# Performance work log

Measured on AMD Instinct MI355X. Metric: run time of the kernel, lower is better.

The kernel has to match this reference:

```python
import jax, jax.numpy as jnp
import numpy as np

TEMPERATURE = 0.5
B, D = 4096, 256

def setup_inputs() -> dict:
    key = jax.random.key(0)
    k1, k2 = jax.random.split(key)
    z_i = jax.random.normal(k1, (B, D), dtype=jnp.float32)
    z_j = jax.random.normal(k2, (B, D), dtype=jnp.float32)
    return {"z_i": z_i, "z_j": z_j}

def reference(z_i, z_j):
    # NT-Xent loss (SimCLR). Cosine similarity of L2-normalized rows == dot product.
    b = z_i.shape[0]
    n = 2 * b
    zi = z_i / jnp.linalg.norm(z_i, axis=1, keepdims=True)
    zj = z_j / jnp.linalg.norm(z_j, axis=1, keepdims=True)
    z = jnp.concatenate([zi, zj], axis=0)            # [N, D]
    sim = jnp.matmul(z, z.T)                          # [N, N] cosine-sim matrix
    # positives: sim(i, i+b) and sim(i+b, i)
    pos = jnp.concatenate([jnp.diagonal(sim, offset=b), jnp.diagonal(sim, offset=-b)])  # [N]
    logits = sim / TEMPERATURE
    # Cross-entropy with the positive as the target class over {pos} U negatives.
    # The candidate set per row is all j != i (the positive j = partner(i) is included,
    # only the self-similarity diagonal is excluded) -> mask diagonal with -inf.
    neg_inf = jnp.asarray(-jnp.inf, dtype=logits.dtype)
    masked = jnp.where(jnp.eye(n, dtype=bool), neg_inf, logits)
    lse = jax.nn.logsumexp(masked, axis=1)            # [N]
    loss = jnp.sum(lse - pos / TEMPERATURE) / n
    return loss
```

## Files before the change

### kernel.cpp

```cpp
#include <hip/hip_runtime.h>
#include <hip/hip_bf16.h>


constexpr int BB = 4096;
constexpr int NN = 8192;
constexpr int DD = 256;
constexpr int TS = 128;
constexpr int NT = NN / TS;
constexpr int NBLK = NT * (NT + 1) / 2;
constexpr int KCH = 64;
constexpr int NCH = DD / KCH;

typedef _Float16 half4v __attribute__((ext_vector_type(4)));
typedef _Float16 half8v __attribute__((ext_vector_type(8)));
typedef float floatx16 __attribute__((ext_vector_type(16)));

__global__ __launch_bounds__(256) void nt_normalize(
    const float* __restrict__ zi, const float* __restrict__ zj,
    _Float16* __restrict__ Z, float* __restrict__ posPartial,
    float* __restrict__ rowsum)
{
    const int lane = threadIdx.x & 63;
    const int wave = threadIdx.x >> 6;
    const int i = blockIdx.x * 4 + wave;

    if (blockIdx.x < 32) rowsum[blockIdx.x * 256 + threadIdx.x] = 0.f;

    const float4 a = ((const float4*)(zi + (size_t)i * DD))[lane];
    const float4 b = ((const float4*)(zj + (size_t)i * DD))[lane];

    float ssi = a.x*a.x + a.y*a.y + a.z*a.z + a.w*a.w;
    float ssj = b.x*b.x + b.y*b.y + b.z*b.z + b.w*b.w;
    float dd  = a.x*b.x + a.y*b.y + a.z*b.z + a.w*b.w;
#pragma unroll
    for (int off = 32; off > 0; off >>= 1) {
        ssi += __shfl_xor(ssi, off);
        ssj += __shfl_xor(ssj, off);
        dd  += __shfl_xor(dd,  off);
    }
    const float invi = rsqrtf(ssi);
    const float invj = rsqrtf(ssj);

    half4v ha, hb;
    ha.x = (_Float16)(a.x * invi); ha.y = (_Float16)(a.y * invi);
    ha.z = (_Float16)(a.z * invi); ha.w = (_Float16)(a.w * invi);
    hb.x = (_Float16)(b.x * invj); hb.y = (_Float16)(b.y * invj);
    hb.z = (_Float16)(b.z * invj); hb.w = (_Float16)(b.w * invj);

    ((half4v*)(Z + (size_t)i * DD))[lane]        = ha;
    ((half4v*)(Z + (size_t)(BB + i) * DD))[lane] = hb;

    __shared__ float ps[4];
    if (lane == 0) ps[wave] = dd * invi * invj;
    __syncthreads();
    if (threadIdx.x == 0)
        posPartial[blockIdx.x] = ps[0] + ps[1] + ps[2] + ps[3];
}

__device__ __forceinline__ float half_sums(float x) {
    int t;
    t = __builtin_amdgcn_update_dpp(0, __builtin_bit_cast(int, x), 0x111, 0xf, 0xf, false);
    x += __builtin_bit_cast(float, t);
    t = __builtin_amdgcn_update_dpp(0, __builtin_bit_cast(int, x), 0x112, 0xf, 0xf, false);
    x += __builtin_bit_cast(float, t);
    t = __builtin_amdgcn_update_dpp(0, __builtin_bit_cast(int, x), 0x114, 0xf, 0xf, false);
    x += __builtin_bit_cast(float, t);
    t = __builtin_amdgcn_update_dpp(0, __builtin_bit_cast(int, x), 0x118, 0xf, 0xf, false);
    x += __builtin_bit_cast(float, t);
    t = __builtin_amdgcn_update_dpp(0, __builtin_bit_cast(int, x), 0x142, 0xa, 0xf, false);
    x += __builtin_bit_cast(float, t);
    return x;
}

__global__ __launch_bounds__(256, 4) void nt_simexp(
    const _Float16* __restrict__ Z, float* __restrict__ rowsum)
{
    __shared__ _Float16 As[TS * KCH];
    __shared__ _Float16 Bs[TS * KCH];
    __shared__ float colacc[TS];

    const int bid = (blockIdx.x & 7) * (NBLK / 8) + (blockIdx.x >> 3);

    int rt = 0, rem = bid;
    while (rem >= NT - rt) { rem -= NT - rt; ++rt; }
    const int ct = rt + rem;
    const bool diag = (rt == ct);

    const int tid = threadIdx.x;
    const int wave = tid >> 6;
    const int lane = tid & 63;
    const int lm = lane & 31;
    const int lh = lane >> 5;
    const int wr = wave >> 1;
    const int wc = wave & 1;

    const int rbase = rt * TS;
    const int cbase = ct * TS;

    if (tid < TS) colacc[tid] = 0.f;

    const int st_row = (lane >> 3);
    const int st_sg  = (lane & 7) ^ (lane >> 3);
    auto stage = [&](const _Float16* srcBase, _Float16* ldsBase, int ch) {
#pragma unroll
        for (int j = 0; j < 4; ++j) {
            const int c = wave * 4 + j;
            const _Float16* g = srcBase + (size_t)(8 * c + st_row) * DD
                                        + ch * KCH + st_sg * 8;
            __builtin_amdgcn_global_load_lds(
                (const __attribute__((address_space(1))) unsigned int*)g,
                (__attribute__((address_space(3))) unsigned int*)(ldsBase + c * 512),
                16, 0, 0);
        }
    };

    floatx16 a00, a01, a10, a11;
#pragma unroll
    for (int r = 0; r < 16; ++r) { a00[r] = 0.f; a01[r] = 0.f; a10[r] = 0.f; a11[r] = 0.f; }

    const _Float16* Ar = Z + (size_t)rbase * DD;
    const _Float16* Br = Z + (size_t)cbase * DD;

    for (int ch = 0; ch < NCH; ++ch) {
        __syncthreads();
        stage(Ar, As, ch);
        stage(Br, Bs, ch);
        asm volatile("s_waitcnt vmcnt(0)" ::: "memory");
        __syncthreads();

#pragma unroll
        for (int s = 0; s < 4; ++s) {
            const int pg = 2 * s + lh;
            const int ph = (pg ^ (lm & 7)) * 8;
            half8v fa0 = *(const half8v*)&As[(wr * 64 + lm) * KCH + ph];
            half8v fa1 = *(const half8v*)&As[(wr * 64 + 32 + lm) * KCH + ph];
            half8v fb0 = *(const half8v*)&Bs[(wc * 64 + lm) * KCH + ph];
            half8v fb1 = *(const half8v*)&Bs[(wc * 64 + 32 + lm) * KCH + ph];
            a00 = __builtin_amdgcn_mfma_f32_32x32x16_f16(fa0, fb0, a00, 0, 0, 0);
            a01 = __builtin_amdgcn_mfma_f32_32x32x16_f16(fa0, fb1, a01, 0, 0, 0);
            a10 = __builtin_amdgcn_mfma_f32_32x32x16_f16(fa1, fb0, a10, 0, 0, 0);
            a11 = __builtin_amdgcn_mfma_f32_32x32x16_f16(fa1, fb1, a11, 0, 0, 0);
        }
    }

    const float KEXP = 2.0f * 1.44269504088896340736f;
    float eb0 = 0.f, eb1 = 0.f;
#pragma unroll
    for (int tr = 0; tr < 2; ++tr) {
#pragma unroll
        for (int r = 0; r < 16; ++r) {
            const int mrow = (r & 3) + 8 * (r >> 2) + 4 * lh;
            float e0 = __builtin_amdgcn_exp2f((tr ? a10[r] : a00[r]) * KEXP);
            float e1 = __builtin_amdgcn_exp2f((tr ? a11[r] : a01[r]) * KEXP);
            if (diag && (wr == wc) && (mrow == lm)) {
                if (tr == 0) e0 = 0.f; else e1 = 0.f;
            }
            if (diag && (wr == wc) && (mrow == lm) && (tr == 1)) e0 = e0;
            eb0 += e0; eb1 += e1;
            if (!diag) {
                float s2 = half_sums(e0 + e1);
                if (lm == 31)
                    atomicAdd(&colacc[wr * 64 + tr * 32 + mrow], s2);
            }
        }
    }


    eb0 += __shfl_xor(eb0, 32);
    eb1 += __shfl_xor(eb1, 32);
    if (lane < 32) {
        atomicAdd(&rowsum[cbase + wc * 64 + lm], eb0);
        atomicAdd(&rowsum[cbase + wc * 64 + 32 + lm], eb1);
    }
    if (!diag) {
        __syncthreads();
        if (tid < TS) atomicAdd(&rowsum[rbase + tid], colacc[tid]);
    }
}

__global__ __launch_bounds__(256) void nt_finalize(
    const float* __restrict__ rowsum, const float* __restrict__ posPartial,
    float* __restrict__ out)
{
    const int tid = threadIdx.x;
    float acc = 0.f;
#pragma unroll
    for (int it = 0; it < NN / 256; ++it)
        acc += __builtin_amdgcn_logf(rowsum[tid + it * 256]);
    float pacc = 0.f;
#pragma unroll
    for (int it = 0; it < 4; ++it)
        pacc += posPartial[tid + it * 256];

#pragma unroll
    for (int off = 32; off > 0; off >>= 1) {
        acc  += __shfl_xor(acc,  off);
        pacc += __shfl_xor(pacc, off);
    }
    __shared__ float sa[4], sp[4];
    const int wave = tid >> 6;
    if ((tid & 63) == 0) { sa[wave] = acc; sp[wave] = pacc; }
    __syncthreads();
    if (tid == 0) {
        const float lntot = (sa[0] + sa[1] + sa[2] + sa[3]) * 0.6931471805599453f;
        const float ptot  = sp[0] + sp[1] + sp[2] + sp[3];
        out[0] = (lntot - 4.0f * ptot) * (1.0f / (float)NN);
    }
}

extern "C" void kernel_launch(void* const* d_in, const int* in_sizes, int n_in,
                              void* d_out, int out_size, void* d_ws, size_t ws_size,
                              hipStream_t stream) {
    const float* zi = (const float*)d_in[0];
    const float* zj = (const float*)d_in[1];
    float* out = (float*)d_out;

    _Float16* Z = (_Float16*)d_ws;
    float* rowsum = (float*)((char*)d_ws + (size_t)NN * DD * 2);
    float* posPartial = rowsum + NN;

    nt_normalize<<<BB / 4, 256, 0, stream>>>(zi, zj, Z, posPartial, rowsum);
    nt_simexp<<<NBLK, 256, 0, stream>>>((const _Float16*)Z, rowsum);
    nt_finalize<<<1, 256, 0, stream>>>(rowsum, posPartial, out);
}
```

Measured before the change: 91.30 us.

## Double-buffer LDS staging with prefetch and closed-form tile indexing

Halves the K chunk to 32 and adds two LDS buffers, so the global-to-LDS loads for the next chunk are issued before the MFMAs on the current chunk. This removes the explicit vmcnt wait and the second barrier per chunk. The serial loop that mapped the block id to a triangular tile becomes a sqrt-based closed form with reversed ordering. MFMA sections are wrapped in s_setprio. There is now no explicit wait on the async LDS loads, so correctness depends on the compiler inserting waitcnts before the LDS reads. Smaller chunks also mean more loop iterations and barriers.

```diff
diff --git a/kernel.cpp b/kernel.cpp
--- a/kernel.cpp
+++ b/kernel.cpp
@@ -8,7 +8,7 @@
 constexpr int TS = 128;
 constexpr int NT = NN / TS;
 constexpr int NBLK = NT * (NT + 1) / 2;
-constexpr int KCH = 64;
+constexpr int KCH = 32;
 constexpr int NCH = DD / KCH;
 
 typedef _Float16 half4v __attribute__((ext_vector_type(4)));
@@ -75,15 +75,17 @@
 __global__ __launch_bounds__(256, 4) void nt_simexp(
     const _Float16* __restrict__ Z, float* __restrict__ rowsum)
 {
-    __shared__ _Float16 As[TS * KCH];
-    __shared__ _Float16 Bs[TS * KCH];
+    __shared__ _Float16 sAB[2][2][TS * KCH];
     __shared__ float colacc[TS];
 
     const int bid = (blockIdx.x & 7) * (NBLK / 8) + (blockIdx.x >> 3);
 
-    int rt = 0, rem = bid;
-    while (rem >= NT - rt) { rem -= NT - rt; ++rt; }
-    const int ct = rt + rem;
+    const int t = NBLK - 1 - bid;
+    int m = (int)((sqrtf((float)(8 * t + 1)) - 1.0f) * 0.5f);
+    while ((m + 1) * (m + 2) / 2 <= t) ++m;
+    while (m * (m + 1) / 2 > t) --m;
+    const int rt = NT - 1 - m;
+    const int ct = NT - 1 - (t - m * (m + 1) / 2);
     const bool diag = (rt == ct);
 
     const int tid = threadIdx.x;
@@ -99,17 +101,25 @@
 
     if (tid < TS) colacc[tid] = 0.f;
 
-    const int st_row = (lane >> 3);
-    const int st_sg  = (lane & 7) ^ (lane >> 3);
-    auto stage = [&](const _Float16* srcBase, _Float16* ldsBase, int ch) {
-#pragma unroll
-        for (int j = 0; j < 4; ++j) {
-            const int c = wave * 4 + j;
-            const _Float16* g = srcBase + (size_t)(8 * c + st_row) * DD
-                                        + ch * KCH + st_sg * 8;
+    const int st_row = lane >> 2;
+    const int st_sg  = (lane & 3) ^ ((lane >> 3) & 3);
+    const _Float16* Ap = Z + (size_t)rbase * DD;
+    const _Float16* Bp = Z + (size_t)cbase * DD;
+
+    auto stage = [&](int buf, int ch) {
+#pragma unroll
+        for (int j = 0; j < 2; ++j) {
+            const int c = wave + 4 * j;
+            const int r = 16 * c + st_row;
+            const _Float16* gA = Ap + (size_t)r * DD + ch * KCH + st_sg * 8;
             __builtin_amdgcn_global_load_lds(
-                (const __attribute__((address_space(1))) unsigned int*)g,
-                (__attribute__((address_space(3))) unsigned int*)(ldsBase + c * 512),
+                (const __attribute__((address_space(1))) unsigned int*)gA,
+                (__attribute__((address_space(3))) unsigned int*)(&sAB[buf][0][c * 512]),
+                16, 0, 0);
+            const _Float16* gB = Bp + (size_t)r * DD + ch * KCH + st_sg * 8;
+            __builtin_amdgcn_global_load_lds(
+                (const __attribute__((address_space(1))) unsigned int*)gB,
+                (__attribute__((address_space(3))) unsigned int*)(&sAB[buf][1][c * 512]),
                 16, 0, 0);
         }
     };
@@ -118,29 +128,28 @@
 #pragma unroll
     for (int r = 0; r < 16; ++r) { a00[r] = 0.f; a01[r] = 0.f; a10[r] = 0.f; a11[r] = 0.f; }
 
-    const _Float16* Ar = Z + (size_t)rbase * DD;
-    const _Float16* Br = Z + (size_t)cbase * DD;
+    stage(0, 0);
 
     for (int ch = 0; ch < NCH; ++ch) {
         __syncthreads();
-        stage(Ar, As, ch);
-        stage(Br, Bs, ch);
-        asm volatile("s_waitcnt vmcnt(0)" ::: "memory");
-        __syncthreads();
-
-#pragma unroll
-        for (int s = 0; s < 4; ++s) {
-            const int pg = 2 * s + lh;
-            const int ph = (pg ^ (lm & 7)) * 8;
-            half8v fa0 = *(const half8v*)&As[(wr * 64 + lm) * KCH + ph];
-            half8v fa1 = *(const half8v*)&As[(wr * 64 + 32 + lm) * KCH + ph];
-            half8v fb0 = *(const half8v*)&Bs[(wc * 64 + lm) * KCH + ph];
-            half8v fb1 = *(const half8v*)&Bs[(wc * 64 + 32 + lm) * KCH + ph];
+        if (ch + 1 < NCH) stage((ch + 1) & 1, ch + 1);
+
+        const int b = ch & 1;
+        __builtin_amdgcn_s_setprio(1);
+#pragma unroll
+        for (int s = 0; s < 2; ++s) {
+            const int pg  = 2 * s + lh;
+            const int ph8 = (pg ^ ((lm >> 1) & 3)) * 8;
+            half8v fa0 = *(const half8v*)&sAB[b][0][(wr * 64 +      lm) * KCH + ph8];
+            half8v fa1 = *(const half8v*)&sAB[b][0][(wr * 64 + 32 + lm) * KCH + ph8];
+            half8v fb0 = *(const half8v*)&sAB[b][1][(wc * 64 +      lm) * KCH + ph8];
+            half8v fb1 = *(const half8v*)&sAB[b][1][(wc * 64 + 32 + lm) * KCH + ph8];
             a00 = __builtin_amdgcn_mfma_f32_32x32x16_f16(fa0, fb0, a00, 0, 0, 0);
             a01 = __builtin_amdgcn_mfma_f32_32x32x16_f16(fa0, fb1, a01, 0, 0, 0);
             a10 = __builtin_amdgcn_mfma_f32_32x32x16_f16(fa1, fb0, a10, 0, 0, 0);
             a11 = __builtin_amdgcn_mfma_f32_32x32x16_f16(fa1, fb1, a11, 0, 0, 0);
         }
+        __builtin_amdgcn_s_setprio(0);
     }
 
     const float KEXP = 2.0f * 1.44269504088896340736f;
@@ -155,7 +164,6 @@
             if (diag && (wr == wc) && (mrow == lm)) {
                 if (tr == 0) e0 = 0.f; else e1 = 0.f;
             }
-            if (diag && (wr == wc) && (mrow == lm) && (tr == 1)) e0 = e0;
             eb0 += e0; eb1 += e1;
             if (!diag) {
                 float s2 = half_sums(e0 + e1);
@@ -164,7 +172,6 @@
             }
         }
     }
-
 
     eb0 += __shfl_xor(eb0, 32);
     eb1 += __shfl_xor(eb1, 32);
```

After: 92.41 us. About the same (+1.2%).
